# Performance work log

Measured on AMD Instinct MI355X. Metric: run time of the kernel, lower is better.

The kernel has to match this reference:

```python
import jax, jax.numpy as jnp
import numpy as np

N, P, EA, EP = 2000, 10000, 60000, 150000
F, K, L = 128, 30, 3
CUTOFF = 4.0
NUM_Z = 119  # len(ase.data.atomic_numbers)


def cosine_cutoff(d, cutoff):
    return jnp.where(d < cutoff, 0.5 * (jnp.cos(jnp.pi * d / cutoff) + 1.0), 0.0)


def sinc_expansion(d, n, cutoff):
    # d: [E,1] -> [E,n]: sin(k*pi*d/cutoff)/d, via normalized sinc
    k = jnp.arange(1, n + 1, dtype=d.dtype)
    return jnp.sinc(d * k / cutoff) * (jnp.pi * k / cutoff)


def mlp2(x, w1, b1, w2, b2):
    return jax.nn.silu(x @ w1 + b1) @ w2 + b2


def painn_update(s, v, U, V, w1, b1, w2, b2):
    Uv = jnp.einsum('nif,fg->nig', v, U)
    Vv = jnp.einsum('nif,fg->nig', v, V)
    Vv_norm = jnp.linalg.norm(Vv, axis=1)  # [n,F]
    a = mlp2(jnp.concatenate([s, Vv_norm], axis=1), w1, b1, w2, b2)  # [n,3F]
    f = s.shape[1]
    a_ss, a_sv, a_vv = a[:, :f], a[:, f:2 * f], a[:, 2 * f:]
    inner = jnp.sum(Uv * Vv, axis=1)  # [n,F]
    return s + a_ss + a_sv * inner, v + a_vv[:, None, :] * Uv


def edge_messages(sender_s, sender_v, edge_state, edge_diff, edge_dist, src,
                  fw, fb, w1, b1, w2, b2, cutoff):
    f = sender_s.shape[1]
    unit = edge_diff / jnp.maximum(jnp.linalg.norm(edge_diff, axis=1, keepdims=True), 1e-12)
    filt = (edge_state @ fw + fb) * cosine_cutoff(edge_dist, cutoff)  # [E,3F]
    out = filt * mlp2(sender_s, w1, b1, w2, b2)[src]  # gather sender scalar features
    g_sv, g_ev, g_ss = out[:, :f], out[:, f:2 * f], out[:, 2 * f:]
    msg_v = sender_v[src] * g_sv[:, None, :] + g_ev[:, None, :] * unit[:, :, None]  # [E,3,F]
    return g_ss, msg_v


def setup_inputs():
    key = jax.random.key(0)
    def nrm(i, shape, scale=0.05):
        return jax.random.normal(jax.random.fold_in(key, i), shape, dtype=jnp.float32) * scale
    atom_xyz = jax.random.uniform(jax.random.fold_in(key, 100), (N, 3), dtype=jnp.float32) * 5.0
    probe_xyz = jax.random.uniform(jax.random.fold_in(key, 101), (P, 3), dtype=jnp.float32) * 5.0
    cell = jnp.eye(3, dtype=jnp.float32) * 5.0 + nrm(102, (3, 3), 0.01)
    nodes_Z = jax.random.randint(jax.random.fold_in(key, 103), (N,), 0, NUM_Z)
    a_src = jax.random.randint(jax.random.fold_in(key, 104), (EA,), 0, N)
    a_dst = (a_src + 1 + jax.random.randint(jax.random.fold_in(key, 105), (EA,), 0, N - 1)) % N  # no self-edges
    atom_edges = jnp.stack([a_src, a_dst], axis=1)
    p_src = jax.random.randint(jax.random.fold_in(key, 106), (EP,), 0, N)
    p_dst = jax.random.randint(jax.random.fold_in(key, 107), (EP,), 0, P)
    probe_edges = jnp.stack([p_src, p_dst], axis=1)
    return dict(
        atom_xyz=atom_xyz, probe_xyz=probe_xyz, cell=cell,
        atom_edges_disp=jnp.zeros((EA, 3), jnp.float32),
        probe_edges_disp=jnp.zeros((EP, 3), jnp.float32),
        atom_embed=nrm(0, (NUM_Z, F), 1.0),
        ai_filter_w=nrm(1, (L, K, 3 * F)), ai_filter_b=nrm(2, (L, 3 * F)),
        ai_w1=nrm(3, (L, F, F)), ai_b1=nrm(4, (L, F)),
        ai_w2=nrm(5, (L, F, 3 * F)), ai_b2=nrm(6, (L, 3 * F)),
        au_U=nrm(7, (L, F, F)), au_V=nrm(8, (L, F, F)),
        au_w1=nrm(9, (L, 2 * F, F)), au_b1=nrm(10, (L, F)),
        au_w2=nrm(11, (L, F, 3 * F)), au_b2=nrm(12, (L, 3 * F)),
        pm_filter_w=nrm(13, (L, K, 3 * F)), pm_filter_b=nrm(14, (L, 3 * F)),
        pm_w1=nrm(15, (L, F, F)), pm_b1=nrm(16, (L, F)),
        pm_w2=nrm(17, (L, F, 3 * F)), pm_b2=nrm(18, (L, 3 * F)),
        pm_gw1=nrm(19, (L, F, 2 * F)), pm_gb1=nrm(20, (L, 2 * F)),
        pm_gw2=nrm(21, (L, 2 * F, 2 * F)), pm_gb2=nrm(22, (L, 2 * F)),
        pu_U=nrm(23, (L, F, F)), pu_V=nrm(24, (L, F, F)),
        pu_w1=nrm(25, (L, 2 * F, F)), pu_b1=nrm(26, (L, F)),
        pu_w2=nrm(27, (L, F, 3 * F)), pu_b2=nrm(28, (L, 3 * F)),
        nodes_Z=nodes_Z, atom_edges=atom_edges, probe_edges=probe_edges,
    )


def reference(atom_xyz, probe_xyz, cell, atom_edges_disp, probe_edges_disp, atom_embed,
              ai_filter_w, ai_filter_b, ai_w1, ai_b1, ai_w2, ai_b2,
              au_U, au_V, au_w1, au_b1, au_w2, au_b2,
              pm_filter_w, pm_filter_b, pm_w1, pm_b1, pm_w2, pm_b2,
              pm_gw1, pm_gb1, pm_gw2, pm_gb2,
              pu_U, pu_V, pu_w1, pu_b1, pu_w2, pu_b2,
              nodes_Z, atom_edges, probe_edges):
    # ---- atom representation model ----
    a_src, a_dst = atom_edges[:, 0], atom_edges[:, 1]
    a_diff = atom_xyz[a_dst] - (atom_xyz[a_src] + atom_edges_disp @ cell)  # [EA,3]
    a_dist = jnp.linalg.norm(a_diff, axis=1, keepdims=True)  # [EA,1]
    a_state = sinc_expansion(a_dist, K, CUTOFF)  # [EA,K]

    s = atom_embed[nodes_Z]  # [N,F]
    v = jnp.zeros((s.shape[0], 3, F), dtype=s.dtype)
    s_list, v_list = [], []
    for l in range(L):
        g_ss, msg_v = edge_messages(s, v, a_state, a_diff, a_dist, a_src,
                                    ai_filter_w[l], ai_filter_b[l], ai_w1[l], ai_b1[l],
                                    ai_w2[l], ai_b2[l], CUTOFF)
        s = s + jax.ops.segment_sum(g_ss, a_dst, num_segments=N)
        v = v + jax.ops.segment_sum(msg_v, a_dst, num_segments=N)
        s, v = painn_update(s, v, au_U[l], au_V[l], au_w1[l], au_b1[l], au_w2[l], au_b2[l])
        s_list.append(s)
        v_list.append(v)

    # ---- probe message model (one-way, gated update) ----
    p_src, p_dst = probe_edges[:, 0], probe_edges[:, 1]
    p_diff = probe_xyz[p_dst] - (atom_xyz[p_src] + probe_edges_disp @ cell)  # [EP,3]
    p_dist = jnp.linalg.norm(p_diff, axis=1, keepdims=True)
    p_state = sinc_expansion(p_dist, K, CUTOFF)

    ps = jnp.zeros((P, F), dtype=s.dtype)
    pv = jnp.zeros((P, 3, F), dtype=s.dtype)
    for l in range(L):
        g_ss, msg_v = edge_messages(s_list[l], v_list[l], p_state, p_diff, p_dist, p_src,
                                    pm_filter_w[l], pm_filter_b[l], pm_w1[l], pm_b1[l],
                                    pm_w2[l], pm_b2[l], CUTOFF)
        m_s = jax.ops.segment_sum(g_ss, p_dst, num_segments=P)
        m_v = jax.ops.segment_sum(msg_v, p_dst, num_segments=P)
        gate = jax.nn.sigmoid(mlp2(m_s, pm_gw1[l], pm_gb1[l], pm_gw2[l], pm_gb2[l]))  # [P,2F]
        gs, gv = gate[:, :F], gate[:, F:]
        ps = ps * gs + (1.0 - gs) * m_s
        pv = pv * gv[:, None, :] + (1.0 - gv[:, None, :]) * m_v
        ps, pv = painn_update(ps, pv, pu_U[l], pu_V[l], pu_w1[l], pu_b1[l], pu_w2[l], pu_b2[l])
    return ps, pv
```

## Files before the change

### kernel.cpp

```cpp
#include <hip/hip_runtime.h>
#include <hip/hip_bf16.h>
#include <math.h>

#define PI_F 3.14159265358979323846f

static constexpr int F = 128;
static constexpr int KB = 30;
static constexpr int LAYERS = 3;
static constexpr float CUT = 4.0f;
static constexpr int BINS = 512;

typedef short bf16x8 __attribute__((ext_vector_type(8)));
typedef float f32x4 __attribute__((ext_vector_type(4)));
typedef unsigned short u16x8 __attribute__((ext_vector_type(8)));

__device__ __forceinline__ float bf2f(unsigned short u) {
    union { unsigned int i; float f; } c; c.i = ((unsigned int)u) << 16; return c.f;
}
__device__ __forceinline__ short f2bf(float x) {
    union { float f; unsigned int u; } c; c.f = x;
    unsigned int r = c.u + 0x7FFFu + ((c.u >> 16) & 1u);
    return (short)(r >> 16);
}

__device__ __forceinline__ float edge_dist(const float* __restrict__ sxyz,
                                           const float* __restrict__ dxyz,
                                           const float* __restrict__ disp,
                                           const float* __restrict__ cell,
                                           int s, int d, int e, float* dx) {
    const float* dp = disp + 3 * (size_t)e;
#pragma unroll
    for (int i = 0; i < 3; i++) {
        float dc = dp[0] * cell[0 * 3 + i] + dp[1] * cell[1 * 3 + i] + dp[2] * cell[2 * 3 + i];
        dx[i] = dxyz[3 * d + i] - (sxyz[3 * s + i] + dc);
    }
    return sqrtf(dx[0] * dx[0] + dx[1] * dx[1] + dx[2] * dx[2]);
}

__global__ void k_count(const int* __restrict__ edges, const float* __restrict__ sxyz,
                        const float* __restrict__ dxyz, const float* __restrict__ disp,
                        const float* __restrict__ cell, int* __restrict__ cnt, int E) {
    int i = blockIdx.x * blockDim.x + threadIdx.x;
    if (i >= E) return;
    int s = edges[2 * i], d = edges[2 * i + 1];
    float dx[3];
    float dist = edge_dist(sxyz, dxyz, disp, cell, s, d, i, dx);
    if (dist < CUT) atomicAdd(&cnt[d], 1);
}

__global__ void k_scan(const int* __restrict__ cnt, int* __restrict__ off, int n) {
    __shared__ int part[1024];
    int t = threadIdx.x;
    int chunk = (n + 1023) / 1024;
    int b = t * chunk; if (b > n) b = n;
    int e = b + chunk; if (e > n) e = n;
    int s = 0;
    for (int i = b; i < e; i++) s += cnt[i];
    part[t] = s;
    __syncthreads();
    for (int o = 1; o < 1024; o <<= 1) {
        int v = part[t];
        int add = (t >= o) ? part[t - o] : 0;
        __syncthreads();
        part[t] = v + add;
        __syncthreads();
    }
    int run = (t == 0) ? 0 : part[t - 1];
    for (int i = b; i < e; i++) { off[i] = run; run += cnt[i]; }
    if (t == 1023) off[n] = part[1023];
}

__global__ void k_scatter(const int* __restrict__ edges, const float* __restrict__ sxyz,
                          const float* __restrict__ dxyz, const float* __restrict__ disp,
                          const float* __restrict__ cell, int* __restrict__ cur,
                          int* __restrict__ eids, int E) {
    int i = blockIdx.x * blockDim.x + threadIdx.x;
    if (i >= E) return;
    int s = edges[2 * i], d = edges[2 * i + 1];
    float dx[3];
    float dist = edge_dist(sxyz, dxyz, disp, cell, s, d, i, dx);
    if (dist < CUT) {
        int pos = atomicAdd(&cur[d], 1);
        eids[pos] = i;
    }
}

__global__ void k_geom_rec(const float* __restrict__ sxyz, const float* __restrict__ dxyz,
                           const float* __restrict__ disp, const float* __restrict__ cell,
                           const int* __restrict__ edges, const int* __restrict__ eids,
                           const int* __restrict__ eoff, int ndst,
                           float4* __restrict__ erec, int* __restrict__ srcs) {
    int pos = blockIdx.x * blockDim.x + threadIdx.x;
    if (pos >= eoff[ndst]) return;
    int e = eids[pos];
    int s = edges[2 * e], d = edges[2 * e + 1];
    float dx[3];
    float dist = edge_dist(sxyz, dxyz, disp, cell, s, d, e, dx);
    float inv = 1.0f / fmaxf(dist, 1e-12f);
    float db = fminf(dist * ((float)BINS / CUT), (float)BINS - 0.0001f);
    erec[pos] = make_float4(dx[0] * inv, dx[1] * inv, dx[2] * inv, db);
    srcs[pos] = s;
}

__global__ void k_sbuild(float* __restrict__ Sp) {
    int i = blockIdx.x * blockDim.x + threadIdx.x;
    if (i > BINS) return;
    float d = (float)i * (CUT / (float)BINS);
    float cc = (d < CUT) ? 0.5f * (cosf(PI_F * d / CUT) + 1.0f) : 0.0f;
    float* row = Sp + (size_t)i * 32;
#pragma unroll
    for (int k = 0; k < KB; k++) {
        float kk = (float)(k + 1);
        float st = (d > 1e-12f) ? sinf(PI_F * d * kk / CUT) / d : PI_F * kk / CUT;
        row[k] = cc * st;
    }
    row[30] = cc;
    row[31] = 0.f;
}

__global__ void k_fwpack(const float* __restrict__ ai_fw, const float* __restrict__ ai_fb,
                         const float* __restrict__ pm_fw, const float* __restrict__ pm_fb,
                         float* __restrict__ fwp) {
    int i = blockIdx.x * blockDim.x + threadIdx.x;
    if (i >= 6 * 32 * 384) return;
    int tbl = i / (32 * 384);
    int k = (i / 384) % 32;
    int c = i % 384;
    const float* fw = (tbl < 3) ? ai_fw + (size_t)tbl * KB * 384 : pm_fw + (size_t)(tbl - 3) * KB * 384;
    const float* fb = (tbl < 3) ? ai_fb + (size_t)tbl * 384 : pm_fb + (size_t)(tbl - 3) * 384;
    float v = 0.f;
    if (k < KB) v = fw[(size_t)k * 384 + c];
    else if (k == 30) v = fb[c];
    fwp[i] = v;
}

__global__ void k_tpack(const short* __restrict__ Tbf, short* __restrict__ Tp) {
    int i = blockIdx.x * blockDim.x + threadIdx.x;
    if (i >= 6 * BINS * 128) return;
    int tbl = i / (BINS * 128);
    int rem = i % (BINS * 128);
    int bin = rem >> 7, lane = rem & 127;
    const short* a = Tbf + ((size_t)tbl * (BINS + 1) + bin) * 512 + lane * 4;
    const short* b = a + 512;
    short* o = Tp + ((size_t)tbl * BINS + bin) * 1024 + lane * 8;
    o[0] = a[0]; o[1] = a[1]; o[2] = a[2]; o[3] = 0;
    o[4] = b[0]; o[5] = b[1]; o[6] = b[2]; o[7] = 0;
}

struct CvtArgs {
    const float* src[14];
    int dstoff[14];
    int Kk[14];
    int Nn[14];
};
__global__ __launch_bounds__(256) void k_cvtw(CvtArgs a, short* __restrict__ dst) {
    int arr = blockIdx.y, l = blockIdx.z;
    int K = a.Kk[arr], N = a.Nn[arr];
    int tilesx = N / 32, tilesy = K / 32;
    int tile = blockIdx.x;
    if (tile >= tilesx * tilesy) return;
    int tn = (tile % tilesx) * 32, tk = (tile / tilesx) * 32;
    __shared__ float tb[32][33];
    int tx = threadIdx.x & 31, ty = threadIdx.x >> 5;
    const float* src = a.src[arr] + (size_t)l * K * N;
    short* d = dst + a.dstoff[arr] + (size_t)l * K * N;
#pragma unroll
    for (int r = 0; r < 4; r++)
        tb[ty * 4 + r][tx] = src[(size_t)(tk + ty * 4 + r) * N + tn + tx];
    __syncthreads();
#pragma unroll
    for (int r = 0; r < 4; r++)
        d[(size_t)(tn + ty * 4 + r) * K + tk + tx] = f2bf(tb[tx][ty * 4 + r]);
}

__global__ void k_embed(const int* __restrict__ Z, const float* __restrict__ emb,
                        float* __restrict__ s, short* __restrict__ sbf, int n) {
    int i = blockIdx.x * blockDim.x + threadIdx.x;
    if (i < n * F) {
        float v = emb[(size_t)Z[i / F] * F + (i % F)];
        s[i] = v; sbf[i] = f2bf(v);
    }
}

__global__ __launch_bounds__(256) void k_gemm(const float* __restrict__ A, const float* __restrict__ B,
                                              void* __restrict__ Cout,
                                              int M, int N, int K, int outmode,
                                              int bstride, int cstride) {
    __shared__ float As[16][64];
    __shared__ float Bs[16][64];
    const float* Bz = B + (size_t)blockIdx.z * bstride;
    int tid = threadIdx.x;
    int bm = blockIdx.y * 64, bn = blockIdx.x * 64;
    int tx = tid & 15, ty = tid >> 4;
    float acc[4][4] = {};
    int arow = tid >> 2;
    int acol = (tid & 3) * 4;
    int brow = tid >> 4;
    int bcol = (tid & 15) * 4;
    for (int k0 = 0; k0 < K; k0 += 16) {
        float4 av = make_float4(0.f, 0.f, 0.f, 0.f);
        int gm = bm + arow;
        if (gm < M) av = *reinterpret_cast<const float4*>(A + (size_t)gm * K + k0 + acol);
        As[acol + 0][arow] = av.x; As[acol + 1][arow] = av.y;
        As[acol + 2][arow] = av.z; As[acol + 3][arow] = av.w;
        float4 bv = *reinterpret_cast<const float4*>(Bz + (size_t)(k0 + brow) * N + bn + bcol);
        Bs[brow][bcol + 0] = bv.x; Bs[brow][bcol + 1] = bv.y;
        Bs[brow][bcol + 2] = bv.z; Bs[brow][bcol + 3] = bv.w;
        __syncthreads();
#pragma unroll
        for (int k = 0; k < 16; k++) {
            float a0 = As[k][ty * 4 + 0], a1 = As[k][ty * 4 + 1];
            float a2 = As[k][ty * 4 + 2], a3 = As[k][ty * 4 + 3];
            float b0 = Bs[k][tx * 4 + 0], b1 = Bs[k][tx * 4 + 1];
            float b2 = Bs[k][tx * 4 + 2], b3 = Bs[k][tx * 4 + 3];
            acc[0][0] += a0 * b0; acc[0][1] += a0 * b1; acc[0][2] += a0 * b2; acc[0][3] += a0 * b3;
            acc[1][0] += a1 * b0; acc[1][1] += a1 * b1; acc[1][2] += a1 * b2; acc[1][3] += a1 * b3;
            acc[2][0] += a2 * b0; acc[2][1] += a2 * b1; acc[2][2] += a2 * b2; acc[2][3] += a2 * b3;
            acc[3][0] += a3 * b0; acc[3][1] += a3 * b1; acc[3][2] += a3 * b2; acc[3][3] += a3 * b3;
        }
        __syncthreads();
    }
#pragma unroll
    for (int i = 0; i < 4; i++) {
        int gm = bm + ty * 4 + i;
        if (gm >= M) continue;
#pragma unroll
        for (int j = 0; j < 4; j++) {
            int gn = bn + tx * 4 + j;
            float v = acc[i][j];
            if (outmode == 0) ((float*)Cout)[(size_t)gm * N + gn] = v;
            else ((short*)Cout)[(size_t)blockIdx.z * cstride + (size_t)gm * 512 + (gn & 127) * 4 + (gn >> 7)] = f2bf(v);
        }
    }
}

__device__ __forceinline__ void mfma_tile_gA(
    const short* __restrict__ A, int arows, int Astride, int row0,
    const short* __restrict__ Bt, int Bstride, int col0, int K,
    int lane, f32x4 acc[4][4]) {
    const int l15 = lane & 15, l16 = lane >> 4;
    for (int k0 = 0; k0 < K; k0 += 32) {
        const int kbase = k0 + l16 * 8;
        bf16x8 af[4], bfr[4];
#pragma unroll
        for (int i = 0; i < 4; i++) {
            int r = row0 + i * 16 + l15;
            bf16x8 t = {};
            if (r < arows) t = *reinterpret_cast<const bf16x8*>(A + (size_t)r * Astride + kbase);
            af[i] = t;
        }
#pragma unroll
        for (int j = 0; j < 4; j++)
            bfr[j] = *reinterpret_cast<const bf16x8*>(Bt + (size_t)(col0 + j * 16 + l15) * Bstride + kbase);
#pragma unroll
        for (int i = 0; i < 4; i++)
#pragma unroll
            for (int j = 0; j < 4; j++)
                acc[i][j] = __builtin_amdgcn_mfma_f32_16x16x32_bf16(af[i], bfr[j], acc[i][j], 0, 0, 0);
    }
}
__device__ __forceinline__ void mfma_tile_lA(
    const short* __restrict__ Alds, int Astride, int lrow0,
    const short* __restrict__ Bt, int Bstride, int col0, int K,
    int lane, f32x4 acc[4][4]) {
    const int l15 = lane & 15, l16 = lane >> 4;
    for (int k0 = 0; k0 < K; k0 += 32) {
        const int kbase = k0 + l16 * 8;
        bf16x8 af[4], bfr[4];
#pragma unroll
        for (int i = 0; i < 4; i++)
            af[i] = *reinterpret_cast<const bf16x8*>(Alds + (size_t)(lrow0 + i * 16 + l15) * Astride + kbase);
#pragma unroll
        for (int j = 0; j < 4; j++)
            bfr[j] = *reinterpret_cast<const bf16x8*>(Bt + (size_t)(col0 + j * 16 + l15) * Bstride + kbase);
#pragma unroll
        for (int i = 0; i < 4; i++)
#pragma unroll
            for (int j = 0; j < 4; j++)
                acc[i][j] = __builtin_amdgcn_mfma_f32_16x16x32_bf16(af[i], bfr[j], acc[i][j], 0, 0, 0);
    }
}

__global__ __launch_bounds__(512) void k_mlp2(
    const short* __restrict__ X, const short* __restrict__ w1t, const float* __restrict__ b1,
    const short* __restrict__ w2t, const float* __restrict__ b2,
    short* __restrict__ PV, int M,
    long xzs, long w1zs, long b1zs, long w2zs, long b2zs, long pvzs) {
    __shared__ short hL[64][136];
    const int z = blockIdx.z;
    const int wave = threadIdx.x >> 6, lane = threadIdx.x & 63;
    const int l15 = lane & 15, l16 = lane >> 4;
    const int rows0 = blockIdx.x * 64;
    const short* Xz = X + (size_t)z * xzs;
    if (wave < 2) {
        f32x4 acc[4][4] = {};
        mfma_tile_gA(Xz, M, 128, rows0, w1t + (size_t)z * w1zs, 128, wave * 64, 128, lane, acc);
        const float* b1z = b1 + (size_t)z * b1zs;
#pragma unroll
        for (int j = 0; j < 4; j++) {
            int cn = wave * 64 + j * 16 + l15;
            float bb = b1z[cn];
#pragma unroll
            for (int i = 0; i < 4; i++)
#pragma unroll
                for (int r = 0; r < 4; r++) {
                    float v = acc[i][j][r] + bb;
                    v = v / (1.0f + expf(-v));
                    hL[i * 16 + l16 * 4 + r][cn] = f2bf(v);
                }
        }
    }
    __syncthreads();
    if (wave < 6) {
        f32x4 acc[4][4] = {};
        mfma_tile_lA(&hL[0][0], 136, 0, w2t + (size_t)z * w2zs, 128, wave * 64, 128, lane, acc);
        const float* b2z = b2 + (size_t)z * b2zs;
        short* PVz = PV + (size_t)z * pvzs;
#pragma unroll
        for (int j = 0; j < 4; j++) {
            int gn = wave * 64 + j * 16 + l15;
            float bb = b2z[gn];
#pragma unroll
            for (int i = 0; i < 4; i++)
#pragma unroll
                for (int r = 0; r < 4; r++) {
                    int gm = rows0 + i * 16 + l16 * 4 + r;
                    if (gm < M)
                        PVz[(size_t)gm * 1024 + (gn & 127) * 8 + (gn >> 7)] = f2bf(acc[i][j][r] + bb);
                }
        }
    }
}

__global__ __launch_bounds__(512) void k_gate(
    const short* __restrict__ ms, const short* __restrict__ mv,
    const short* __restrict__ g1t, const float* __restrict__ gb1,
    const short* __restrict__ g2t, const float* __restrict__ gb2,
    float* __restrict__ ps, float* __restrict__ pv, short* __restrict__ pvb, int P) {
    __shared__ short hL[64][264];
    __shared__ short gL[64][264];
    const int wave = threadIdx.x >> 6, lane = threadIdx.x & 63;
    const int l15 = lane & 15, l16 = lane >> 4;
    const int rows0 = blockIdx.x * 64;
    if (wave < 4) {
        f32x4 acc[4][4] = {};
        mfma_tile_gA(ms, P, 128, rows0, g1t, 128, wave * 64, 128, lane, acc);
#pragma unroll
        for (int j = 0; j < 4; j++) {
            int cn = wave * 64 + j * 16 + l15;
            float bb = gb1[cn];
#pragma unroll
            for (int i = 0; i < 4; i++)
#pragma unroll
                for (int r = 0; r < 4; r++) {
                    float v = acc[i][j][r] + bb;
                    v = v / (1.0f + expf(-v));
                    hL[i * 16 + l16 * 4 + r][cn] = f2bf(v);
                }
        }
    }
    __syncthreads();
    if (wave < 4) {
        f32x4 acc[4][4] = {};
        mfma_tile_lA(&hL[0][0], 264, 0, g2t, 256, wave * 64, 256, lane, acc);
#pragma unroll
        for (int j = 0; j < 4; j++) {
            int cn = wave * 64 + j * 16 + l15;
            float bb = gb2[cn];
#pragma unroll
            for (int i = 0; i < 4; i++)
#pragma unroll
                for (int r = 0; r < 4; r++) {
                    float v = acc[i][j][r] + bb;
                    gL[i * 16 + l16 * 4 + r][cn] = f2bf(1.0f / (1.0f + expf(-v)));
                }
        }
    }
    __syncthreads();
    for (int it = 0; it < 16; it++) {
        int idx = it * 512 + threadIdx.x;
        int r = idx >> 7, g = idx & 127;
        int row = rows0 + r;
        if (row >= P) continue;
        float gs = bf2f(gL[r][g]);
        float gv = bf2f(gL[r][128 + g]);
        size_t o = (size_t)row * 128 + g;
        ps[o] = ps[o] * gs + (1.0f - gs) * bf2f(ms[o]);
#pragma unroll
        for (int i3 = 0; i3 < 3; i3++) {
            size_t o3 = ((size_t)row * 3 + i3) * 128 + g;
            float val = pv[o3] * gv + (1.0f - gv) * bf2f(mv[o3]);
            pv[o3] = val;
            pvb[o3] = f2bf(val);
        }
    }
}

__global__ __launch_bounds__(512) void k_paiupd(
    const short* __restrict__ Avv,
    const float* __restrict__ s_in,
    const float* __restrict__ v_in,
    const short* __restrict__ Ut, const short* __restrict__ Vt,
    const short* __restrict__ w1t, const float* __restrict__ b1,
    const short* __restrict__ w2t, const float* __restrict__ b2,
    float* __restrict__ s_out, float* __restrict__ v_out,
    short* __restrict__ s_out_bf, short* __restrict__ v_out_pk,
    short* __restrict__ abuf, int n) {
    __shared__ short UvL[192][136];
    __shared__ short VvL[192][136];
    __shared__ short catL[64][264];
    __shared__ short hL[64][136];
    const int wave = threadIdx.x >> 6, lane = threadIdx.x & 63;
    const int l15 = lane & 15, l16 = lane >> 4;
    const int rows0 = blockIdx.x * 64;
    const int vr0 = rows0 * 3;
    if (wave < 6) {
        const int chunk = wave % 3;
        const short* Bt = (wave < 3) ? Ut : Vt;
        f32x4 acc[4][4] = {};
        mfma_tile_gA(Avv, 3 * n, 128, vr0 + chunk * 64, Bt, 128, 0, 128, lane, acc);
        short (*dst)[136] = (wave < 3) ? UvL : VvL;
#pragma unroll
        for (int j = 0; j < 4; j++) {
            int cn = j * 16 + l15;
#pragma unroll
            for (int i = 0; i < 4; i++)
#pragma unroll
                for (int r = 0; r < 4; r++)
                    dst[chunk * 64 + i * 16 + l16 * 4 + r][cn] = f2bf(acc[i][j][r]);
        }
        f32x4 acc2[4][4] = {};
        mfma_tile_gA(Avv, 3 * n, 128, vr0 + chunk * 64, Bt, 128, 64, 128, lane, acc2);
#pragma unroll
        for (int j = 0; j < 4; j++) {
            int cn = 64 + j * 16 + l15;
#pragma unroll
            for (int i = 0; i < 4; i++)
#pragma unroll
                for (int r = 0; r < 4; r++)
                    dst[chunk * 64 + i * 16 + l16 * 4 + r][cn] = f2bf(acc2[i][j][r]);
        }
    }
    __syncthreads();
    for (int it = 0; it < 16; it++) {
        int idx = it * 512 + threadIdx.x;
        int r = idx >> 7, g = idx & 127;
        int row = rows0 + r;
        float sv = (row < n) ? s_in[(size_t)row * 128 + g] : 0.f;
        float w0 = bf2f(VvL[3 * r + 0][g]);
        float w1 = bf2f(VvL[3 * r + 1][g]);
        float w2 = bf2f(VvL[3 * r + 2][g]);
        catL[r][g] = f2bf(sv);
        catL[r][128 + g] = f2bf(sqrtf(w0 * w0 + w1 * w1 + w2 * w2));
    }
    __syncthreads();
    if (wave < 2) {
        f32x4 acc[4][4] = {};
        mfma_tile_lA(&catL[0][0], 264, 0, w1t, 256, wave * 64, 256, lane, acc);
#pragma unroll
        for (int j = 0; j < 4; j++) {
            int cn = wave * 64 + j * 16 + l15;
            float bb = b1[cn];
#pragma unroll
            for (int i = 0; i < 4; i++)
#pragma unroll
                for (int r = 0; r < 4; r++) {
                    float v = acc[i][j][r] + bb;
                    v = v / (1.0f + expf(-v));
                    hL[i * 16 + l16 * 4 + r][cn] = f2bf(v);
                }
        }
    }
    __syncthreads();
    if (wave < 6) {
        f32x4 acc[4][4] = {};
        mfma_tile_lA(&hL[0][0], 136, 0, w2t, 128, wave * 64, 128, lane, acc);
#pragma unroll
        for (int j = 0; j < 4; j++) {
            int gn = wave * 64 + j * 16 + l15;
            float bb = b2[gn];
#pragma unroll
            for (int i = 0; i < 4; i++)
#pragma unroll
                for (int r = 0; r < 4; r++) {
                    int gm = rows0 + i * 16 + l16 * 4 + r;
                    if (gm < n) abuf[(size_t)gm * 384 + gn] = f2bf(acc[i][j][r] + bb);
                }
        }
    }
    __threadfence_block();
    __syncthreads();
    for (int it = 0; it < 16; it++) {
        int idx = it * 512 + threadIdx.x;
        int r = idx >> 7, g = idx & 127;
        int row = rows0 + r;
        if (row >= n) continue;
        float u0 = bf2f(UvL[3 * r + 0][g]);
        float u1 = bf2f(UvL[3 * r + 1][g]);
        float u2 = bf2f(UvL[3 * r + 2][g]);
        float w0 = bf2f(VvL[3 * r + 0][g]);
        float w1 = bf2f(VvL[3 * r + 1][g]);
        float w2 = bf2f(VvL[3 * r + 2][g]);
        float inner = u0 * w0 + u1 * w1 + u2 * w2;
        const short* arow = abuf + (size_t)row * 384;
        float ass = bf2f(arow[g]), asv = bf2f(arow[128 + g]), avv = bf2f(arow[256 + g]);
        size_t so = (size_t)row * 128 + g;
        float snew = s_in[so] + ass + asv * inner;
        s_out[so] = snew;
        if (s_out_bf) s_out_bf[so] = f2bf(snew);
        size_t b = (size_t)row * 384;
        float r0 = v_in[b + g] + avv * u0;
        float r1 = v_in[b + 128 + g] + avv * u1;
        float r2 = v_in[b + 256 + g] + avv * u2;
        v_out[b + g] = r0;
        v_out[b + 128 + g] = r1;
        v_out[b + 256 + g] = r2;
        if (v_out_pk) {
            size_t pb = (size_t)row * 1024 + (size_t)g * 8;
            v_out_pk[pb + 4] = f2bf(r0);
            v_out_pk[pb + 5] = f2bf(r1);
            v_out_pk[pb + 6] = f2bf(r2);
        }
    }
}

__global__ __launch_bounds__(256) void k_gather(
    const float4* __restrict__ erec, const int* __restrict__ srcs,
    const int* __restrict__ eoff, const short* __restrict__ Tp,
    const short* __restrict__ PV,
    const float* __restrict__ s_in, const float* __restrict__ v_in,
    float* __restrict__ s_out, float* __restrict__ v_out,
    short* __restrict__ s_out_bf, short* __restrict__ v_out_bf, int ndst,
    long tzs, long pvzs, long mszs, long mvzs) {
    const int t = threadIdx.x & 127;
    const int half = threadIdx.x >> 7;
    const int z = blockIdx.z;
    const short* __restrict__ T = Tp + (size_t)z * tzs;
    const short* __restrict__ PVz = PV + (size_t)z * pvzs;
    short* __restrict__ msz = s_out_bf ? s_out_bf + (size_t)z * mszs : nullptr;
    short* __restrict__ mvz = v_out_bf ? v_out_bf + (size_t)z * mvzs : nullptr;

    for (int d = blockIdx.x * 2 + half; d < ndst; d += gridDim.x * 2) {
        const int e0 = eoff[d], e1 = eoff[d + 1];
        float accs = 0.f, av0 = 0.f, av1 = 0.f, av2 = 0.f;

        auto ACC = [&](const float4& u, int bin, u16x8 Tv, u16x8 Pv) {
            const float fr = u.w - (float)bin;
            const float f0 = fmaf(fr, bf2f(Tv[4]) - bf2f(Tv[0]), bf2f(Tv[0]));
            const float f1 = fmaf(fr, bf2f(Tv[5]) - bf2f(Tv[1]), bf2f(Tv[1]));
            const float f2 = fmaf(fr, bf2f(Tv[6]) - bf2f(Tv[2]), bf2f(Tv[2]));
            const float gsv = f0 * bf2f(Pv[0]);
            const float gev = f1 * bf2f(Pv[1]);
            accs += f2 * bf2f(Pv[2]);
            av0 = fmaf(bf2f(Pv[4]), gsv, fmaf(gev, u.x, av0));
            av1 = fmaf(bf2f(Pv[5]), gsv, fmaf(gev, u.y, av1));
            av2 = fmaf(bf2f(Pv[6]), gsv, fmaf(gev, u.z, av2));
        };

        int ii = e0;
        for (; ii + 3 < e1; ii += 4) {
            const float4 u0 = erec[ii + 0], u1 = erec[ii + 1];
            const float4 u2 = erec[ii + 2], u3 = erec[ii + 3];
            const int s0 = srcs[ii + 0], s1 = srcs[ii + 1];
            const int s2 = srcs[ii + 2], s3 = srcs[ii + 3];
            const int b0 = (int)u0.w, b1 = (int)u1.w, b2 = (int)u2.w, b3 = (int)u3.w;
            const u16x8 T0 = *(const u16x8*)(T + ((size_t)b0 * 128 + t) * 8);
            const u16x8 T1 = *(const u16x8*)(T + ((size_t)b1 * 128 + t) * 8);
            const u16x8 T2 = *(const u16x8*)(T + ((size_t)b2 * 128 + t) * 8);
            const u16x8 T3 = *(const u16x8*)(T + ((size_t)b3 * 128 + t) * 8);
            const u16x8 P0 = *(const u16x8*)(PVz + ((size_t)s0 * 128 + t) * 8);
            const u16x8 P1 = *(const u16x8*)(PVz + ((size_t)s1 * 128 + t) * 8);
            const u16x8 P2 = *(const u16x8*)(PVz + ((size_t)s2 * 128 + t) * 8);
            const u16x8 P3 = *(const u16x8*)(PVz + ((size_t)s3 * 128 + t) * 8);
            ACC(u0, b0, T0, P0); ACC(u1, b1, T1, P1);
            ACC(u2, b2, T2, P2); ACC(u3, b3, T3, P3);
        }
        for (; ii < e1; ++ii) {
            const float4 u = erec[ii];
            const int s = srcs[ii];
            const int b = (int)u.w;
            const u16x8 Tv = *(const u16x8*)(T + ((size_t)b * 128 + t) * 8);
            const u16x8 Pv = *(const u16x8*)(PVz + ((size_t)s * 128 + t) * 8);
            ACC(u, b, Tv, Pv);
        }

        if (s_in) {
            accs += s_in[(size_t)d * 128 + t];
            av0 += v_in[(size_t)d * 384 + t];
            av1 += v_in[(size_t)d * 384 + 128 + t];
            av2 += v_in[(size_t)d * 384 + 256 + t];
        }
        if (s_out) {
            s_out[(size_t)d * 128 + t] = accs;
            v_out[(size_t)d * 384 + t] = av0;
            v_out[(size_t)d * 384 + 128 + t] = av1;
            v_out[(size_t)d * 384 + 256 + t] = av2;
        }
        if (msz) msz[(size_t)d * 128 + t] = f2bf(accs);
        if (mvz) {
            mvz[(size_t)(3 * d + 0) * 128 + t] = f2bf(av0);
            mvz[(size_t)(3 * d + 1) * 128 + t] = f2bf(av1);
            mvz[(size_t)(3 * d + 2) * 128 + t] = f2bf(av2);
        }
    }
}

extern "C" void kernel_launch(void* const* d_in, const int* in_sizes, int n_in,
                              void* d_out, int out_size, void* d_ws, size_t ws_size,
                              hipStream_t stream) {
    const float* atom_xyz  = (const float*)d_in[0];
    const float* probe_xyz = (const float*)d_in[1];
    const float* cell      = (const float*)d_in[2];
    const float* a_disp    = (const float*)d_in[3];
    const float* p_disp    = (const float*)d_in[4];
    const float* atom_embed= (const float*)d_in[5];
    const float* ai_fw = (const float*)d_in[6];
    const float* ai_fb = (const float*)d_in[7];
    const float* ai_b1 = (const float*)d_in[9];
    const float* ai_b2 = (const float*)d_in[11];
    const float* au_b1 = (const float*)d_in[15];
    const float* au_b2 = (const float*)d_in[17];
    const float* pm_fw = (const float*)d_in[18];
    const float* pm_fb = (const float*)d_in[19];
    const float* pm_b1 = (const float*)d_in[21];
    const float* pm_b2 = (const float*)d_in[23];
    const float* pm_gb1= (const float*)d_in[25];
    const float* pm_gb2= (const float*)d_in[27];
    const float* pu_b1 = (const float*)d_in[31];
    const float* pu_b2 = (const float*)d_in[33];
    const int* nodes_Z = (const int*)d_in[34];
    const int* a_edges = (const int*)d_in[35];
    const int* p_edges = (const int*)d_in[36];

    const int N  = in_sizes[34];
    const int EA = in_sizes[35] / 2;
    const int EP = in_sizes[36] / 2;
    const int P  = in_sizes[1] / 3;

    enum { W_AI_W1=0, W_AI_W2, W_AU_U, W_AU_V, W_AU_W1, W_AU_W2, W_PM_W1, W_PM_W2,
           W_PM_GW1, W_PM_GW2, W_PU_U, W_PU_V, W_PU_W1, W_PU_W2 };
    const int wsrc[14] = {8,10,12,13,14,16,20,22,24,26,28,29,30,32};
    const int wK[14]   = {128,128,128,128,256,128,128,128,128,256,128,128,256,128};
    const int wN[14]   = {128,384,128,128,128,384,128,384,256,256,128,128,128,384};
    size_t woff[15]; woff[0] = 0;
    for (int i = 0; i < 14; i++) woff[i + 1] = woff[i] + (size_t)3 * wK[i] * wN[i];

    char* w = (char*)d_ws;
    size_t off = 0;
    auto alloc = [&](size_t bytes) -> void* {
        void* p = w + off;
        off = (off + bytes + 255) & ~(size_t)255;
        return p;
    };
    int* a_off  = (int*)alloc((size_t)(N + 1) * 4);
    int* a_cur  = (int*)alloc((size_t)N * 4);
    int* a_eids = (int*)alloc((size_t)EA * 4);
    int* a_srcs = (int*)alloc((size_t)EA * 4);
    int* p_off  = (int*)alloc((size_t)(P + 1) * 4);
    int* p_cur  = (int*)alloc((size_t)P * 4);
    int* p_eids = (int*)alloc((size_t)EP * 4);
    int* p_srcs = (int*)alloc((size_t)EP * 4);
    float4* a_erec = (float4*)alloc((size_t)EA * 16);
    float4* p_erec = (float4*)alloc((size_t)EP * 16);
    float* Sp   = (float*)alloc((size_t)(BINS + 1) * 32 * 4);
    float* fwp  = (float*)alloc((size_t)6 * 32 * 384 * 4);
    short* Tbf  = (short*)alloc((size_t)6 * (BINS + 1) * 512 * 2);
    short* Tp   = (short*)alloc((size_t)6 * BINS * 1024 * 2);
    short* wbt  = (short*)alloc(woff[14] * 2);
    float* s0     = (float*)alloc((size_t)N * F * 4);
    float* v0     = (float*)alloc((size_t)N * 3 * F * 4);
    float* s_list = (float*)alloc((size_t)LAYERS * N * F * 4);
    float* v_list = (float*)alloc((size_t)LAYERS * N * 3 * F * 4);
    float* msf    = (float*)alloc((size_t)N * F * 4);
    float* mvf    = (float*)alloc((size_t)N * 3 * F * 4);
    short* s0_bf    = (short*)alloc((size_t)N * F * 2);
    short* sbf_list = (short*)alloc((size_t)LAYERS * N * F * 2);
    short* vpk8     = (short*)alloc((size_t)4 * N * 1024 * 2);
    short* ms3      = (short*)alloc((size_t)3 * P * F * 2);
    short* mv3      = (short*)alloc((size_t)3 * 3 * P * F * 2);
    short* mv_bf    = (short*)alloc((size_t)N * 3 * F * 2);
    short* abuf_bf  = (short*)alloc((size_t)P * 3 * F * 2);
    short* pv_bf    = (short*)alloc((size_t)P * 3 * F * 2);
    (void)ws_size; (void)n_in;

    hipMemsetAsync(a_cur, 0, (size_t)N * 4, stream);
    k_count<<<(EA + 255) / 256, 256, 0, stream>>>(a_edges, atom_xyz, atom_xyz, a_disp, cell, a_cur, EA);
    k_scan<<<1, 1024, 0, stream>>>(a_cur, a_off, N);
    hipMemcpyAsync(a_cur, a_off, (size_t)N * 4, hipMemcpyDeviceToDevice, stream);
    k_scatter<<<(EA + 255) / 256, 256, 0, stream>>>(a_edges, atom_xyz, atom_xyz, a_disp, cell, a_cur, a_eids, EA);
    hipMemsetAsync(p_cur, 0, (size_t)P * 4, stream);
    k_count<<<(EP + 255) / 256, 256, 0, stream>>>(p_edges, atom_xyz, probe_xyz, p_disp, cell, p_cur, EP);
    k_scan<<<1, 1024, 0, stream>>>(p_cur, p_off, P);
    hipMemcpyAsync(p_cur, p_off, (size_t)P * 4, hipMemcpyDeviceToDevice, stream);
    k_scatter<<<(EP + 255) / 256, 256, 0, stream>>>(p_edges, atom_xyz, probe_xyz, p_disp, cell, p_cur, p_eids, EP);

    k_geom_rec<<<(EA + 255) / 256, 256, 0, stream>>>(atom_xyz, atom_xyz, a_disp, cell, a_edges,
                                                     a_eids, a_off, N, a_erec, a_srcs);
    k_geom_rec<<<(EP + 255) / 256, 256, 0, stream>>>(atom_xyz, probe_xyz, p_disp, cell, p_edges,
                                                     p_eids, p_off, P, p_erec, p_srcs);

    k_sbuild<<<(BINS + 256) / 256, 256, 0, stream>>>(Sp);
    k_fwpack<<<(6 * 32 * 384 + 255) / 256, 256, 0, stream>>>(ai_fw, ai_fb, pm_fw, pm_fb, fwp);
    {
        dim3 g(384 / 64, (BINS + 1 + 63) / 64, 6);
        k_gemm<<<g, 256, 0, stream>>>(Sp, fwp, Tbf, BINS + 1, 384, 32, 4, 32 * 384, (BINS + 1) * 512);
    }
    k_tpack<<<(6 * BINS * 128 + 255) / 256, 256, 0, stream>>>(Tbf, Tp);

    {
        CvtArgs ca;
        for (int i = 0; i < 14; i++) {
            ca.src[i] = (const float*)d_in[wsrc[i]];
            ca.dstoff[i] = (int)woff[i];
            ca.Kk[i] = wK[i]; ca.Nn[i] = wN[i];
        }
        k_cvtw<<<dim3(64, 14, 3), 256, 0, stream>>>(ca, wbt);
    }
    auto wt = [&](int a, int l) { return wbt + woff[a] + (size_t)l * wK[a] * wN[a]; };

    k_embed<<<(N * F + 255) / 256, 256, 0, stream>>>(nodes_Z, atom_embed, s0, s0_bf, N);
    hipMemsetAsync(v0, 0, (size_t)N * 3 * F * 4, stream);
    hipMemsetAsync(vpk8, 0, (size_t)N * 1024 * 2, stream);

    auto pvbuf = [&](int idx) { return vpk8 + (size_t)idx * N * 1024; };
    const int nb_atom = (N + 63) / 64;
    const int nb_probe = (P + 63) / 64;

    for (int l = 0; l < LAYERS; l++) {
        const float* scur = l ? (s_list + (size_t)(l - 1) * N * F) : s0;
        const float* vcur = l ? (v_list + (size_t)(l - 1) * N * 3 * F) : v0;
        const short* scur_bf = l ? (sbf_list + (size_t)(l - 1) * N * F) : s0_bf;
        k_mlp2<<<dim3(nb_atom, 1, 1), 512, 0, stream>>>(
            scur_bf, wt(W_AI_W1, l), ai_b1 + (size_t)l * F,
            wt(W_AI_W2, l), ai_b2 + (size_t)l * 3 * F,
            pvbuf(l), N, 0, 0, 0, 0, 0, 0);
        k_gather<<<dim3((N + 1) / 2, 1, 1), 256, 0, stream>>>(a_erec, a_srcs, a_off,
                 Tp + (size_t)l * BINS * 1024, pvbuf(l),
                 scur, vcur, msf, mvf, nullptr, mv_bf, N, 0, 0, 0, 0);
        k_paiupd<<<dim3(nb_atom), 512, 0, stream>>>(
            mv_bf, msf, mvf,
            wt(W_AU_U, l), wt(W_AU_V, l),
            wt(W_AU_W1, l), au_b1 + (size_t)l * F,
            wt(W_AU_W2, l), au_b2 + (size_t)l * 3 * F,
            s_list + (size_t)l * N * F, v_list + (size_t)l * N * 3 * F,
            sbf_list + (size_t)l * N * F, pvbuf(l + 1), abuf_bf, N);
    }

    float* ps = (float*)d_out;
    float* pv = (float*)d_out + (size_t)P * F;
    hipMemsetAsync(d_out, 0, (size_t)out_size * 4, stream);

    k_mlp2<<<dim3(nb_atom, 1, 3), 512, 0, stream>>>(
        sbf_list, wt(W_PM_W1, 0), pm_b1, wt(W_PM_W2, 0), pm_b2,
        pvbuf(1), N,
        (long)N * F, (long)128 * 128, 128, (long)128 * 384, 384, (long)N * 1024);

    k_gather<<<dim3((P + 1) / 2, 1, 3), 256, 0, stream>>>(p_erec, p_srcs, p_off,
             Tp + (size_t)3 * BINS * 1024, pvbuf(1),
             nullptr, nullptr, nullptr, nullptr, ms3, mv3, P,
             (long)BINS * 1024, (long)N * 1024, (long)P * F, (long)3 * P * F);

    for (int l = 0; l < LAYERS; l++) {
        k_gate<<<dim3(nb_probe), 512, 0, stream>>>(
            ms3 + (size_t)l * P * F, mv3 + (size_t)l * 3 * P * F,
            wt(W_PM_GW1, l), pm_gb1 + (size_t)l * 2 * F,
            wt(W_PM_GW2, l), pm_gb2 + (size_t)l * 2 * F,
            ps, pv, pv_bf, P);
        k_paiupd<<<dim3(nb_probe), 512, 0, stream>>>(
            pv_bf, ps, pv,
            wt(W_PU_U, l), wt(W_PU_V, l),
            wt(W_PU_W1, l), pu_b1 + (size_t)l * F,
            wt(W_PU_W2, l), pu_b2 + (size_t)l * 3 * F,
            ps, pv, nullptr, nullptr, abuf_bf, P);
    }
}
```

Before: 715.5 us.

## Fuse probe gate and PaiNN update into one kernel; split gather edges across threads

Merges the probe gating kernel and the probe PaiNN update kernel into a single per-tile kernel. The gated vector state now stays in shared memory as bf16 instead of making a round trip through a global pv_bf buffer, and one launch per layer is removed. The gather kernel now runs 512 threads per block: two threads work on each destination/feature pair, each taking half of the edge range, and their partial sums are combined through shared memory. This gives more parallelism and latency hiding on high-degree nodes, at the cost of a barrier and larger shared-memory and register use.

```diff
diff --git a/kernel.cpp b/kernel.cpp
--- a/kernel.cpp
+++ b/kernel.cpp
@@ -332,70 +332,6 @@
     }
 }
 
-__global__ __launch_bounds__(512) void k_gate(
-    const short* __restrict__ ms, const short* __restrict__ mv,
-    const short* __restrict__ g1t, const float* __restrict__ gb1,
-    const short* __restrict__ g2t, const float* __restrict__ gb2,
-    float* __restrict__ ps, float* __restrict__ pv, short* __restrict__ pvb, int P) {
-    __shared__ short hL[64][264];
-    __shared__ short gL[64][264];
-    const int wave = threadIdx.x >> 6, lane = threadIdx.x & 63;
-    const int l15 = lane & 15, l16 = lane >> 4;
-    const int rows0 = blockIdx.x * 64;
-    if (wave < 4) {
-        f32x4 acc[4][4] = {};
-        mfma_tile_gA(ms, P, 128, rows0, g1t, 128, wave * 64, 128, lane, acc);
-#pragma unroll
-        for (int j = 0; j < 4; j++) {
-            int cn = wave * 64 + j * 16 + l15;
-            float bb = gb1[cn];
-#pragma unroll
-            for (int i = 0; i < 4; i++)
-#pragma unroll
-                for (int r = 0; r < 4; r++) {
-                    float v = acc[i][j][r] + bb;
-                    v = v / (1.0f + expf(-v));
-                    hL[i * 16 + l16 * 4 + r][cn] = f2bf(v);
-                }
-        }
-    }
-    __syncthreads();
-    if (wave < 4) {
-        f32x4 acc[4][4] = {};
-        mfma_tile_lA(&hL[0][0], 264, 0, g2t, 256, wave * 64, 256, lane, acc);
-#pragma unroll
-        for (int j = 0; j < 4; j++) {
-            int cn = wave * 64 + j * 16 + l15;
-            float bb = gb2[cn];
-#pragma unroll
-            for (int i = 0; i < 4; i++)
-#pragma unroll
-                for (int r = 0; r < 4; r++) {
-                    float v = acc[i][j][r] + bb;
-                    gL[i * 16 + l16 * 4 + r][cn] = f2bf(1.0f / (1.0f + expf(-v)));
-                }
-        }
-    }
-    __syncthreads();
-    for (int it = 0; it < 16; it++) {
-        int idx = it * 512 + threadIdx.x;
-        int r = idx >> 7, g = idx & 127;
-        int row = rows0 + r;
-        if (row >= P) continue;
-        float gs = bf2f(gL[r][g]);
-        float gv = bf2f(gL[r][128 + g]);
-        size_t o = (size_t)row * 128 + g;
-        ps[o] = ps[o] * gs + (1.0f - gs) * bf2f(ms[o]);
-#pragma unroll
-        for (int i3 = 0; i3 < 3; i3++) {
-            size_t o3 = ((size_t)row * 3 + i3) * 128 + g;
-            float val = pv[o3] * gv + (1.0f - gv) * bf2f(mv[o3]);
-            pv[o3] = val;
-            pvb[o3] = f2bf(val);
-        }
-    }
-}
-
 __global__ __launch_bounds__(512) void k_paiupd(
     const short* __restrict__ Avv,
     const float* __restrict__ s_in,
@@ -417,28 +353,20 @@
     if (wave < 6) {
         const int chunk = wave % 3;
         const short* Bt = (wave < 3) ? Ut : Vt;
-        f32x4 acc[4][4] = {};
-        mfma_tile_gA(Avv, 3 * n, 128, vr0 + chunk * 64, Bt, 128, 0, 128, lane, acc);
         short (*dst)[136] = (wave < 3) ? UvL : VvL;
 #pragma unroll
-        for (int j = 0; j < 4; j++) {
-            int cn = j * 16 + l15;
-#pragma unroll
-            for (int i = 0; i < 4; i++)
-#pragma unroll
-                for (int r = 0; r < 4; r++)
-                    dst[chunk * 64 + i * 16 + l16 * 4 + r][cn] = f2bf(acc[i][j][r]);
-        }
-        f32x4 acc2[4][4] = {};
-        mfma_tile_gA(Avv, 3 * n, 128, vr0 + chunk * 64, Bt, 128, 64, 128, lane, acc2);
-#pragma unroll
-        for (int j = 0; j < 4; j++) {
-            int cn = 64 + j * 16 + l15;
-#pragma unroll
-            for (int i = 0; i < 4; i++)
-#pragma unroll
-                for (int r = 0; r < 4; r++)
-                    dst[chunk * 64 + i * 16 + l16 * 4 + r][cn] = f2bf(acc2[i][j][r]);
+        for (int half = 0; half < 2; half++) {
+            f32x4 acc[4][4] = {};
+            mfma_tile_gA(Avv, 3 * n, 128, vr0 + chunk * 64, Bt, 128, half * 64, 128, lane, acc);
+#pragma unroll
+            for (int j = 0; j < 4; j++) {
+                int cn = half * 64 + j * 16 + l15;
+#pragma unroll
+                for (int i = 0; i < 4; i++)
+#pragma unroll
+                    for (int r = 0; r < 4; r++)
+                        dst[chunk * 64 + i * 16 + l16 * 4 + r][cn] = f2bf(acc[i][j][r]);
+            }
         }
     }
     __syncthreads();
@@ -524,7 +452,172 @@
     }
 }
 
-__global__ __launch_bounds__(256) void k_gather(
+__global__ __launch_bounds__(512) void k_probe_layer(
+    const short* __restrict__ ms, const short* __restrict__ mv,
+    const short* __restrict__ g1t, const float* __restrict__ gb1,
+    const short* __restrict__ g2t, const float* __restrict__ gb2,
+    const short* __restrict__ Ut, const short* __restrict__ Vt,
+    const short* __restrict__ w1t, const float* __restrict__ b1,
+    const short* __restrict__ w2t, const float* __restrict__ b2,
+    float* __restrict__ ps, float* __restrict__ pv,
+    short* __restrict__ abuf, int P) {
+    __shared__ short S0[192 * 136];
+    __shared__ short S1[192 * 136];
+    __shared__ short S2[192 * 136];
+    const int tid = threadIdx.x;
+    const int wave = tid >> 6, lane = tid & 63;
+    const int l15 = lane & 15, l16 = lane >> 4;
+    const int rows0 = blockIdx.x * 64;
+    if (wave < 4) {
+        f32x4 acc[4][4] = {};
+        mfma_tile_gA(ms, P, 128, rows0, g1t, 128, wave * 64, 128, lane, acc);
+#pragma unroll
+        for (int j = 0; j < 4; j++) {
+            int cn = wave * 64 + j * 16 + l15;
+            float bb = gb1[cn];
+#pragma unroll
+            for (int i = 0; i < 4; i++)
+#pragma unroll
+                for (int r = 0; r < 4; r++) {
+                    float v = acc[i][j][r] + bb;
+                    v = v / (1.0f + expf(-v));
+                    S0[(i * 16 + l16 * 4 + r) * 264 + cn] = f2bf(v);
+                }
+        }
+    }
+    __syncthreads();
+    if (wave < 4) {
+        f32x4 acc[4][4] = {};
+        mfma_tile_lA(S0, 264, 0, g2t, 256, wave * 64, 256, lane, acc);
+#pragma unroll
+        for (int j = 0; j < 4; j++) {
+            int cn = wave * 64 + j * 16 + l15;
+            float bb = gb2[cn];
+#pragma unroll
+            for (int i = 0; i < 4; i++)
+#pragma unroll
+                for (int r = 0; r < 4; r++) {
+                    float v = acc[i][j][r] + bb;
+                    S1[(i * 16 + l16 * 4 + r) * 264 + cn] = f2bf(1.0f / (1.0f + expf(-v)));
+                }
+        }
+    }
+    __syncthreads();
+    for (int it = 0; it < 16; it++) {
+        int idx = it * 512 + tid;
+        int r = idx >> 7, g = idx & 127;
+        int row = rows0 + r;
+        if (row < P) {
+            float gs = bf2f(S1[r * 264 + g]);
+            float gv = bf2f(S1[r * 264 + 128 + g]);
+            size_t o = (size_t)row * 128 + g;
+            ps[o] = ps[o] * gs + (1.0f - gs) * bf2f(ms[o]);
+#pragma unroll
+            for (int i3 = 0; i3 < 3; i3++) {
+                size_t o3 = ((size_t)row * 3 + i3) * 128 + g;
+                float val = pv[o3] * gv + (1.0f - gv) * bf2f(mv[o3]);
+                pv[o3] = val;
+                S2[(3 * r + i3) * 136 + g] = f2bf(val);
+            }
+        } else {
+#pragma unroll
+            for (int i3 = 0; i3 < 3; i3++) S2[(3 * r + i3) * 136 + g] = 0;
+        }
+    }
+    __threadfence_block();
+    __syncthreads();
+    if (wave < 6) {
+        const int chunk = wave % 3;
+        const short* Bt = (wave < 3) ? Ut : Vt;
+        short* dst = (wave < 3) ? S0 : S1;
+#pragma unroll
+        for (int half = 0; half < 2; half++) {
+            f32x4 acc[4][4] = {};
+            mfma_tile_lA(S2, 136, chunk * 64, Bt, 128, half * 64, 128, lane, acc);
+#pragma unroll
+            for (int j = 0; j < 4; j++) {
+                int cn = half * 64 + j * 16 + l15;
+#pragma unroll
+                for (int i = 0; i < 4; i++)
+#pragma unroll
+                    for (int r = 0; r < 4; r++)
+                        dst[(chunk * 64 + i * 16 + l16 * 4 + r) * 136 + cn] = f2bf(acc[i][j][r]);
+            }
+        }
+    }
+    __syncthreads();
+    for (int it = 0; it < 16; it++) {
+        int idx = it * 512 + tid;
+        int r = idx >> 7, g = idx & 127;
+        int row = rows0 + r;
+        float sv = (row < P) ? ps[(size_t)row * 128 + g] : 0.f;
+        float w0 = bf2f(S1[(3 * r + 0) * 136 + g]);
+        float w1 = bf2f(S1[(3 * r + 1) * 136 + g]);
+        float w2 = bf2f(S1[(3 * r + 2) * 136 + g]);
+        S2[r * 264 + g] = f2bf(sv);
+        S2[r * 264 + 128 + g] = f2bf(sqrtf(w0 * w0 + w1 * w1 + w2 * w2));
+    }
+    __syncthreads();
+    if (wave < 2) {
+        f32x4 acc[4][4] = {};
+        mfma_tile_lA(S2, 264, 0, w1t, 256, wave * 64, 256, lane, acc);
+#pragma unroll
+        for (int j = 0; j < 4; j++) {
+            int cn = wave * 64 + j * 16 + l15;
+            float bb = b1[cn];
+#pragma unroll
+            for (int i = 0; i < 4; i++)
+#pragma unroll
+                for (int r = 0; r < 4; r++) {
+                    float v = acc[i][j][r] + bb;
+                    v = v / (1.0f + expf(-v));
+                    S2[16896 + (i * 16 + l16 * 4 + r) * 136 + cn] = f2bf(v);
+                }
+        }
+    }
+    __syncthreads();
+    if (wave < 6) {
+        f32x4 acc[4][4] = {};
+        mfma_tile_lA(S2 + 16896, 136, 0, w2t, 128, wave * 64, 128, lane, acc);
+#pragma unroll
+        for (int j = 0; j < 4; j++) {
+            int gn = wave * 64 + j * 16 + l15;
+            float bb = b2[gn];
+#pragma unroll
+            for (int i = 0; i < 4; i++)
+#pragma unroll
+                for (int r = 0; r < 4; r++) {
+                    int gm = rows0 + i * 16 + l16 * 4 + r;
+                    if (gm < P) abuf[(size_t)gm * 384 + gn] = f2bf(acc[i][j][r] + bb);
+                }
+        }
+    }
+    __threadfence_block();
+    __syncthreads();
+    for (int it = 0; it < 16; it++) {
+        int idx = it * 512 + tid;
+        int r = idx >> 7, g = idx & 127;
+        int row = rows0 + r;
+        if (row >= P) continue;
+        float u0 = bf2f(S0[(3 * r + 0) * 136 + g]);
+        float u1 = bf2f(S0[(3 * r + 1) * 136 + g]);
+        float u2 = bf2f(S0[(3 * r + 2) * 136 + g]);
+        float w0 = bf2f(S1[(3 * r + 0) * 136 + g]);
+        float w1 = bf2f(S1[(3 * r + 1) * 136 + g]);
+        float w2 = bf2f(S1[(3 * r + 2) * 136 + g]);
+        float inner = u0 * w0 + u1 * w1 + u2 * w2;
+        const short* arow = abuf + (size_t)row * 384;
+        float ass = bf2f(arow[g]), asv = bf2f(arow[128 + g]), avv = bf2f(arow[256 + g]);
+        size_t so = (size_t)row * 128 + g;
+        ps[so] = ps[so] + ass + asv * inner;
+        size_t b = (size_t)row * 384;
+        pv[b + g] += avv * u0;
+        pv[b + 128 + g] += avv * u1;
+        pv[b + 256 + g] += avv * u2;
+    }
+}
+
+__global__ __launch_bounds__(512) void k_gather(
     const float4* __restrict__ erec, const int* __restrict__ srcs,
     const int* __restrict__ eoff, const short* __restrict__ Tp,
     const short* __restrict__ PV,
@@ -532,58 +625,77 @@
     float* __restrict__ s_out, float* __restrict__ v_out,
     short* __restrict__ s_out_bf, short* __restrict__ v_out_bf, int ndst,
     long tzs, long pvzs, long mszs, long mvzs) {
-    const int t = threadIdx.x & 127;
-    const int half = threadIdx.x >> 7;
+    __shared__ float red[2][128][4];
+    const int tid = threadIdx.x;
+    const int t = tid & 127;
+    const int split = (tid >> 7) & 1;
+    const int dsel = tid >> 8;
     const int z = blockIdx.z;
     const short* __restrict__ T = Tp + (size_t)z * tzs;
     const short* __restrict__ PVz = PV + (size_t)z * pvzs;
     short* __restrict__ msz = s_out_bf ? s_out_bf + (size_t)z * mszs : nullptr;
     short* __restrict__ mvz = v_out_bf ? v_out_bf + (size_t)z * mvzs : nullptr;
 
-    for (int d = blockIdx.x * 2 + half; d < ndst; d += gridDim.x * 2) {
-        const int e0 = eoff[d], e1 = eoff[d + 1];
-        float accs = 0.f, av0 = 0.f, av1 = 0.f, av2 = 0.f;
-
-        auto ACC = [&](const float4& u, int bin, u16x8 Tv, u16x8 Pv) {
-            const float fr = u.w - (float)bin;
-            const float f0 = fmaf(fr, bf2f(Tv[4]) - bf2f(Tv[0]), bf2f(Tv[0]));
-            const float f1 = fmaf(fr, bf2f(Tv[5]) - bf2f(Tv[1]), bf2f(Tv[1]));
-            const float f2 = fmaf(fr, bf2f(Tv[6]) - bf2f(Tv[2]), bf2f(Tv[2]));
-            const float gsv = f0 * bf2f(Pv[0]);
-            const float gev = f1 * bf2f(Pv[1]);
-            accs += f2 * bf2f(Pv[2]);
-            av0 = fmaf(bf2f(Pv[4]), gsv, fmaf(gev, u.x, av0));
-            av1 = fmaf(bf2f(Pv[5]), gsv, fmaf(gev, u.y, av1));
-            av2 = fmaf(bf2f(Pv[6]), gsv, fmaf(gev, u.z, av2));
-        };
-
-        int ii = e0;
-        for (; ii + 3 < e1; ii += 4) {
-            const float4 u0 = erec[ii + 0], u1 = erec[ii + 1];
-            const float4 u2 = erec[ii + 2], u3 = erec[ii + 3];
-            const int s0 = srcs[ii + 0], s1 = srcs[ii + 1];
-            const int s2 = srcs[ii + 2], s3 = srcs[ii + 3];
-            const int b0 = (int)u0.w, b1 = (int)u1.w, b2 = (int)u2.w, b3 = (int)u3.w;
-            const u16x8 T0 = *(const u16x8*)(T + ((size_t)b0 * 128 + t) * 8);
-            const u16x8 T1 = *(const u16x8*)(T + ((size_t)b1 * 128 + t) * 8);
-            const u16x8 T2 = *(const u16x8*)(T + ((size_t)b2 * 128 + t) * 8);
-            const u16x8 T3 = *(const u16x8*)(T + ((size_t)b3 * 128 + t) * 8);
-            const u16x8 P0 = *(const u16x8*)(PVz + ((size_t)s0 * 128 + t) * 8);
-            const u16x8 P1 = *(const u16x8*)(PVz + ((size_t)s1 * 128 + t) * 8);
-            const u16x8 P2 = *(const u16x8*)(PVz + ((size_t)s2 * 128 + t) * 8);
-            const u16x8 P3 = *(const u16x8*)(PVz + ((size_t)s3 * 128 + t) * 8);
-            ACC(u0, b0, T0, P0); ACC(u1, b1, T1, P1);
-            ACC(u2, b2, T2, P2); ACC(u3, b3, T3, P3);
-        }
-        for (; ii < e1; ++ii) {
-            const float4 u = erec[ii];
-            const int s = srcs[ii];
-            const int b = (int)u.w;
-            const u16x8 Tv = *(const u16x8*)(T + ((size_t)b * 128 + t) * 8);
-            const u16x8 Pv = *(const u16x8*)(PVz + ((size_t)s * 128 + t) * 8);
-            ACC(u, b, Tv, Pv);
-        }
-
+    const int d = blockIdx.x * 2 + dsel;
+    const bool valid = d < ndst;
+    int e0 = 0, e1 = 0;
+    if (valid) { e0 = eoff[d]; e1 = eoff[d + 1]; }
+    const int emid = e0 + ((e1 - e0 + 1) >> 1);
+    const int lo = split ? emid : e0;
+    const int hi = split ? e1 : emid;
+
+    float accs = 0.f, av0 = 0.f, av1 = 0.f, av2 = 0.f;
+
+    auto ACC = [&](const float4& u, int bin, u16x8 Tv, u16x8 Pv) {
+        const float fr = u.w - (float)bin;
+        const float f0 = fmaf(fr, bf2f(Tv[4]) - bf2f(Tv[0]), bf2f(Tv[0]));
+        const float f1 = fmaf(fr, bf2f(Tv[5]) - bf2f(Tv[1]), bf2f(Tv[1]));
+        const float f2 = fmaf(fr, bf2f(Tv[6]) - bf2f(Tv[2]), bf2f(Tv[2]));
+        const float gsv = f0 * bf2f(Pv[0]);
+        const float gev = f1 * bf2f(Pv[1]);
+        accs += f2 * bf2f(Pv[2]);
+        av0 = fmaf(bf2f(Pv[4]), gsv, fmaf(gev, u.x, av0));
+        av1 = fmaf(bf2f(Pv[5]), gsv, fmaf(gev, u.y, av1));
+        av2 = fmaf(bf2f(Pv[6]), gsv, fmaf(gev, u.z, av2));
+    };
+
+    int ii = lo;
+    for (; ii + 3 < hi; ii += 4) {
+        const float4 u0 = erec[ii + 0], u1 = erec[ii + 1];
+        const float4 u2 = erec[ii + 2], u3 = erec[ii + 3];
+        const int s0 = srcs[ii + 0], s1 = srcs[ii + 1];
+        const int s2 = srcs[ii + 2], s3 = srcs[ii + 3];
+        const int b0 = (int)u0.w, b1 = (int)u1.w, b2 = (int)u2.w, b3 = (int)u3.w;
+        const u16x8 T0 = *(const u16x8*)(T + ((size_t)b0 * 128 + t) * 8);
+        const u16x8 T1 = *(const u16x8*)(T + ((size_t)b1 * 128 + t) * 8);
+        const u16x8 T2 = *(const u16x8*)(T + ((size_t)b2 * 128 + t) * 8);
+        const u16x8 T3 = *(const u16x8*)(T + ((size_t)b3 * 128 + t) * 8);
+        const u16x8 P0 = *(const u16x8*)(PVz + ((size_t)s0 * 128 + t) * 8);
+        const u16x8 P1 = *(const u16x8*)(PVz + ((size_t)s1 * 128 + t) * 8);
+        const u16x8 P2 = *(const u16x8*)(PVz + ((size_t)s2 * 128 + t) * 8);
+        const u16x8 P3 = *(const u16x8*)(PVz + ((size_t)s3 * 128 + t) * 8);
+        ACC(u0, b0, T0, P0); ACC(u1, b1, T1, P1);
+        ACC(u2, b2, T2, P2); ACC(u3, b3, T3, P3);
+    }
+    for (; ii < hi; ++ii) {
+        const float4 u = erec[ii];
+        const int s = srcs[ii];
+        const int b = (int)u.w;
+        const u16x8 Tv = *(const u16x8*)(T + ((size_t)b * 128 + t) * 8);
+        const u16x8 Pv = *(const u16x8*)(PVz + ((size_t)s * 128 + t) * 8);
+        ACC(u, b, Tv, Pv);
+    }
+
+    if (split) {
+        red[dsel][t][0] = accs; red[dsel][t][1] = av0;
+        red[dsel][t][2] = av1;  red[dsel][t][3] = av2;
+    }
+    __syncthreads();
+    if (!split && valid) {
+        accs += red[dsel][t][0];
+        av0 += red[dsel][t][1];
+        av1 += red[dsel][t][2];
+        av2 += red[dsel][t][3];
         if (s_in) {
             accs += s_in[(size_t)d * 128 + t];
             av0 += v_in[(size_t)d * 384 + t];
@@ -680,7 +792,6 @@
     short* mv3      = (short*)alloc((size_t)3 * 3 * P * F * 2);
     short* mv_bf    = (short*)alloc((size_t)N * 3 * F * 2);
     short* abuf_bf  = (short*)alloc((size_t)P * 3 * F * 2);
-    short* pv_bf    = (short*)alloc((size_t)P * 3 * F * 2);
     (void)ws_size; (void)n_in;
 
     hipMemsetAsync(a_cur, 0, (size_t)N * 4, stream);
@@ -734,7 +845,7 @@
             scur_bf, wt(W_AI_W1, l), ai_b1 + (size_t)l * F,
             wt(W_AI_W2, l), ai_b2 + (size_t)l * 3 * F,
             pvbuf(l), N, 0, 0, 0, 0, 0, 0);
-        k_gather<<<dim3((N + 1) / 2, 1, 1), 256, 0, stream>>>(a_erec, a_srcs, a_off,
+        k_gather<<<dim3((N + 1) / 2, 1, 1), 512, 0, stream>>>(a_erec, a_srcs, a_off,
                  Tp + (size_t)l * BINS * 1024, pvbuf(l),
                  scur, vcur, msf, mvf, nullptr, mv_bf, N, 0, 0, 0, 0);
         k_paiupd<<<dim3(nb_atom), 512, 0, stream>>>(
@@ -755,22 +866,19 @@
         pvbuf(1), N,
         (long)N * F, (long)128 * 128, 128, (long)128 * 384, 384, (long)N * 1024);
 
-    k_gather<<<dim3((P + 1) / 2, 1, 3), 256, 0, stream>>>(p_erec, p_srcs, p_off,
+    k_gather<<<dim3((P + 1) / 2, 1, 3), 512, 0, stream>>>(p_erec, p_srcs, p_off,
              Tp + (size_t)3 * BINS * 1024, pvbuf(1),
              nullptr, nullptr, nullptr, nullptr, ms3, mv3, P,
              (long)BINS * 1024, (long)N * 1024, (long)P * F, (long)3 * P * F);
 
     for (int l = 0; l < LAYERS; l++) {
-        k_gate<<<dim3(nb_probe), 512, 0, stream>>>(
+        k_probe_layer<<<dim3(nb_probe), 512, 0, stream>>>(
             ms3 + (size_t)l * P * F, mv3 + (size_t)l * 3 * P * F,
             wt(W_PM_GW1, l), pm_gb1 + (size_t)l * 2 * F,
             wt(W_PM_GW2, l), pm_gb2 + (size_t)l * 2 * F,
-            ps, pv, pv_bf, P);
-        k_paiupd<<<dim3(nb_probe), 512, 0, stream>>>(
-            pv_bf, ps, pv,
             wt(W_PU_U, l), wt(W_PU_V, l),
             wt(W_PU_W1, l), pu_b1 + (size_t)l * F,
             wt(W_PU_W2, l), pu_b2 + (size_t)l * 3 * F,
-            ps, pv, nullptr, nullptr, abuf_bf, P);
-    }
-}
+            ps, pv, abuf_bf, P);
+    }
+}
```

Measured after the change: 711.9 us. Within noise of the previous version (-0.5%).
